# Optimization experiments

Hardware: AMD Instinct MI355X
Metric: run time of the kernel (lower is better)

The kernel has to match this reference:

```python
import jax, jax.numpy as jnp
import numpy as np

H = 32       # num_attention_heads
KV = 8       # num_key_value_heads
D = 128      # head_dim
HID = 4096   # hidden_size
EPS = 1e-6   # rms_norm_eps
BASE = 1000000.0  # rope_theta


def setup_inputs() -> dict:
    key = jax.random.key(0)
    ks = jax.random.split(key, 5)
    B, S = 1, 2048
    s = 0.02
    return {
        "x": jax.random.normal(ks[0], (B, S, HID), jnp.float32),
        "wq": jax.random.normal(ks[1], (H * D, HID), jnp.float32) * s,
        "wk": jax.random.normal(ks[2], (KV * D, HID), jnp.float32) * s,
        "wv": jax.random.normal(ks[3], (KV * D, HID), jnp.float32) * s,
        "wo": jax.random.normal(ks[4], (HID, H * D), jnp.float32) * s,
        "q_norm_w": jnp.ones((D,), jnp.float32),
        "k_norm_w": jnp.ones((D,), jnp.float32),
    }


def _rms(x, w):
    # F.rms_norm over last dim (head_dim), computed in fp32 then cast back
    x32 = x.astype(jnp.float32)
    y = x32 * jax.lax.rsqrt(jnp.mean(x32 * x32, axis=-1, keepdims=True) + EPS)
    return (y * w.astype(jnp.float32)).astype(x.dtype)


def _rope_tables(S, dtype):
    pair = jnp.arange(0, D, 2, dtype=jnp.float32)
    theta = 1.0 / (BASE ** (pair / D))                       # [D/2]
    ang = jnp.arange(S, dtype=jnp.float32)[:, None] * theta  # [S, D/2]
    ang = jnp.concatenate([ang, ang], axis=-1)               # [S, D]
    return jnp.cos(ang).astype(dtype), jnp.sin(ang).astype(dtype)


def _rope(x, cos, sin):
    # x: [B, H, S, D]; rotate_half convention (cat of two halves)
    half = D // 2
    rot = jnp.concatenate([-x[..., half:], x[..., :half]], axis=-1)
    return x * cos + rot * sin


def reference(x, wq, wk, wv, wo, q_norm_w, k_norm_w):
    B, S, _ = x.shape
    q = (x @ wq.T).reshape(B, S, H, D)
    k = (x @ wk.T).reshape(B, S, KV, D)
    v = (x @ wv.T).reshape(B, S, KV, D)
    q = _rms(q, q_norm_w).transpose(0, 2, 1, 3)   # [B, H, S, D]
    k = _rms(k, k_norm_w).transpose(0, 2, 1, 3)   # [B, KV, S, D]
    v = v.transpose(0, 2, 1, 3)                   # [B, KV, S, D]
    cos, sin = _rope_tables(S, x.dtype)
    q = _rope(q, cos, sin)
    k = _rope(k, cos, sin)
    # GQA: group Q heads over KV heads, causal SDPA
    G = H // KV
    qg = q.reshape(B, KV, G, S, D)
    scale = 1.0 / np.sqrt(D).astype(np.float32)
    scores = jnp.einsum('bkgsd,bktd->bkgst', qg, k) * scale  # [B,KV,G,S,S]
    causal = jnp.tril(jnp.ones((S, S), dtype=bool))
    scores = jnp.where(causal, scores, jnp.asarray(-jnp.inf, scores.dtype))
    p = jax.nn.softmax(scores, axis=-1)
    out = jnp.einsum('bkgst,bktd->bkgsd', p, v)               # [B,KV,G,S,D]
    out = out.reshape(B, H, S, D).transpose(0, 2, 1, 3).reshape(B, S, H * D)
    return out @ wo.T
```

## Files before the change

### kernel.cpp

```cpp
#include <hip/hip_runtime.h>
#include <hip/hip_bf16.h>

#define S_LEN   2048
#define HID_SZ  4096
#define NH      32
#define NKV     8
#define HD      128
#define EPS_F   1e-6f
#define QSCALE  0.1275174475f

typedef __attribute__((ext_vector_type(8))) short bf16x8;
typedef __attribute__((ext_vector_type(4))) float f32x4;

#define AS1(p) ((__attribute__((address_space(1))) void*)(p))
#define AS3(p) ((__attribute__((address_space(3))) void*)(p))

__device__ __forceinline__ short f2b(float f) {
  unsigned u = __builtin_bit_cast(unsigned, f);
  unsigned r = (u + 0x7fffu + ((u >> 16) & 1u)) >> 16;
  return (short)(unsigned short)r;
}
__device__ __forceinline__ float b2f(short s) {
  return __builtin_bit_cast(float, (unsigned)((unsigned short)s) << 16);
}

__global__ __launch_bounds__(256) void cvt_f32_bf16(const float* __restrict__ in,
                                                    short* __restrict__ out, int n4) {
  int i = blockIdx.x * 256 + threadIdx.x;
  if (i >= n4) return;
  float4 f = reinterpret_cast<const float4*>(in)[i];
  short4 o;
  o.x = f2b(f.x); o.y = f2b(f.y); o.z = f2b(f.z); o.w = f2b(f.w);
  reinterpret_cast<short4*>(out)[i] = o;
}

__global__ void rope_tables_k(float* __restrict__ cosT, float* __restrict__ sinT) {
  int s = blockIdx.x;
  int j = threadIdx.x;
  float theta = exp2f(-(float)(2 * j) * (19.931568569324174f / 128.0f));
  float ang = (float)s * theta;
  float sv, cv;
  sincosf(ang, &sv, &cv);
  cosT[s * 64 + j] = cv;
  sinT[s * 64 + j] = sv;
}

__global__ __launch_bounds__(256)
void rmsrope_k(const short* __restrict__ src, int srcCol,
               const float* __restrict__ w,
               const float* __restrict__ cosT, const float* __restrict__ sinT,
               short* __restrict__ dst, int heads, float outScale) {
  int gw   = blockIdx.x * 4 + (threadIdx.x >> 6);
  int lane = threadIdx.x & 63;
  int s = gw / heads;
  int h = gw - s * heads;
  const short* p = src + (size_t)s * 6144 + srcCol + h * HD;
  float x0 = b2f(p[lane]), x1 = b2f(p[lane + 64]);
  float ss = x0 * x0 + x1 * x1;
#pragma unroll
  for (int off = 1; off < 64; off <<= 1) ss += __shfl_xor(ss, off);
  float r = rsqrtf(ss * (1.0f / 128.0f) + EPS_F);
  float y0 = x0 * r * w[lane];
  float y1 = x1 * r * w[lane + 64];
  float c = cosT[s * 64 + lane], sn = sinT[s * 64 + lane];
  float o0 = (y0 * c - y1 * sn) * outScale;
  float o1 = (y1 * c + y0 * sn) * outScale;
  short* d = dst + ((size_t)h * S_LEN + s) * HD;
  d[lane]      = f2b(o0);
  d[lane + 64] = f2b(o1);
}

__global__ __launch_bounds__(256)
void vtrans_k(const short* __restrict__ qkvb, short* __restrict__ vt) {
  __shared__ short t[64][65];
  int s0 = blockIdx.x * 64;
  int d0 = blockIdx.y * 64;
  int kv = blockIdx.z;
  int j  = threadIdx.x & 63;
  int i0 = threadIdx.x >> 6;
#pragma unroll
  for (int r = 0; r < 16; ++r) {
    int i = i0 * 16 + r;
    t[i][j] = qkvb[(size_t)(s0 + i) * 6144 + 5120 + kv * HD + d0 + j];
  }
  __syncthreads();
#pragma unroll
  for (int r = 0; r < 16; ++r) {
    int i = i0 * 16 + r;
    vt[((size_t)kv * HD + d0 + i) * S_LEN + s0 + j] = t[j][i];
  }
}

template<bool BF16OUT>
__global__ __launch_bounds__(256)
void gemm_bt_k(const short* __restrict__ A, const short* __restrict__ B,
               void* __restrict__ Cv, int M, int N, int K) {
  __shared__ short As[128 * 32];
  __shared__ short Bs[128 * 32];
  int tid  = threadIdx.x;
  int lane = tid & 63;
  int wave = tid >> 6;
  int wr = wave >> 1, wc = wave & 1;
  int m0 = blockIdx.y * 128, n0 = blockIdx.x * 128;
  f32x4 acc[4][4] = {};
  int row16 = lane & 15;
  int kg    = (lane >> 4) << 3;
  int c0 = tid, c1 = tid + 256;
  const size_t rA0 = (size_t)(m0 + (c0 >> 2)) * K + ((c0 & 3) << 3);
  const size_t rA1 = (size_t)(m0 + (c1 >> 2)) * K + ((c1 & 3) << 3);
  const size_t rB0 = (size_t)(n0 + (c0 >> 2)) * K + ((c0 & 3) << 3);
  const size_t rB1 = (size_t)(n0 + (c1 >> 2)) * K + ((c1 & 3) << 3);
  for (int kt = 0; kt < K; kt += 32) {
    __builtin_amdgcn_global_load_lds(AS1(A + rA0 + kt), AS3(&As[c0 * 8]), 16, 0, 0);
    __builtin_amdgcn_global_load_lds(AS1(A + rA1 + kt), AS3(&As[c1 * 8]), 16, 0, 0);
    __builtin_amdgcn_global_load_lds(AS1(B + rB0 + kt), AS3(&Bs[c0 * 8]), 16, 0, 0);
    __builtin_amdgcn_global_load_lds(AS1(B + rB1 + kt), AS3(&Bs[c1 * 8]), 16, 0, 0);
    __syncthreads();
    bf16x8 af[4], bf[4];
#pragma unroll
    for (int i = 0; i < 4; ++i)
      af[i] = *reinterpret_cast<const bf16x8*>(&As[(wr * 64 + i * 16 + row16) * 32 + kg]);
#pragma unroll
    for (int j = 0; j < 4; ++j)
      bf[j] = *reinterpret_cast<const bf16x8*>(&Bs[(wc * 64 + j * 16 + row16) * 32 + kg]);
#pragma unroll
    for (int i = 0; i < 4; ++i)
#pragma unroll
      for (int j = 0; j < 4; ++j)
        acc[i][j] = __builtin_amdgcn_mfma_f32_16x16x32_bf16(af[i], bf[j], acc[i][j], 0, 0, 0);
    __syncthreads();
  }
  int rsub = (lane >> 4) << 2;
#pragma unroll
  for (int i = 0; i < 4; ++i)
#pragma unroll
    for (int j = 0; j < 4; ++j) {
      size_t base = (size_t)(m0 + wr * 64 + i * 16 + rsub) * N + (n0 + wc * 64 + j * 16 + row16);
#pragma unroll
      for (int reg = 0; reg < 4; ++reg) {
        if constexpr (BF16OUT) ((short*)Cv)[base + (size_t)reg * N] = f2b(acc[i][j][reg]);
        else                   ((float*)Cv)[base + (size_t)reg * N] = acc[i][j][reg];
      }
    }
}

__global__ __launch_bounds__(256)
void attn_k(const short* __restrict__ Qr, const short* __restrict__ Kr,
            const short* __restrict__ Vt, short* __restrict__ Ob) {
  constexpr int PP = 72;
  __shared__ short Kl[2][64 * 128];
  __shared__ short Vl[2][128 * 64];
  __shared__ short Pl[4][16 * PP];
  int pr  = blockIdx.x;
  int h   = blockIdx.y;
  int kvh = h >> 2;
  int tid = threadIdx.x, wave = tid >> 6, lane = tid & 63;
  int row16 = lane & 15, kg = (lane >> 4) << 3, rsub = (lane >> 4) << 2;
  int colb  = (lane >> 4) << 4;
  int swz   = (row16 & 7) << 4;

  const short* Kb = Kr + (size_t)kvh * S_LEN * HD;
  const short* Vb = Vt + (size_t)kvh * HD * S_LEN;

  int kso[4], vso[4], llo[4];
#pragma unroll
  for (int r = 0; r < 4; ++r) {
    int c = tid + r * 256;
    llo[r] = c * 8;
    int krow = c >> 4, ch = c & 15;
    int sch = (ch & 8) | ((ch ^ krow) & 7);
    kso[r] = krow * HD + sch * 8;
    int dr = c >> 3, vch = c & 7;
    int vsch = (vch ^ dr) & 7;
    vso[r] = dr * S_LEN + vsch * 8;
  }

#define STAGE(BUF, KT) do {                                                      \
    const short* Kt_ = Kb + (size_t)(KT) * 64 * HD;                              \
    const short* Vt_ = Vb + (KT) * 64;                                           \
    _Pragma("unroll")                                                            \
    for (int r_ = 0; r_ < 4; ++r_)                                               \
      __builtin_amdgcn_global_load_lds(AS1(Kt_ + kso[r_]),                       \
                                       AS3(&Kl[BUF][llo[r_]]), 16, 0, 0);        \
    _Pragma("unroll")                                                            \
    for (int r_ = 0; r_ < 4; ++r_)                                               \
      __builtin_amdgcn_global_load_lds(AS1(Vt_ + vso[r_]),                       \
                                       AS3(&Vl[BUF][llo[r_]]), 16, 0, 0);        \
  } while (0)

  STAGE(0, 0);

  for (int half = 0; half < 2; ++half) {
    int qb = half ? pr : (31 - pr);
    int qrow0 = qb * 64 + wave * 16;

    bf16x8 qf[4];
    {
      const short* qp = Qr + ((size_t)h * S_LEN + qrow0 + row16) * HD + kg;
#pragma unroll
      for (int ks = 0; ks < 4; ++ks)
        qf[ks] = *reinterpret_cast<const bf16x8*>(qp + ks * 32);
    }
    f32x4 o[8] = {};
    float mrow[4], lrow[4];
#pragma unroll
    for (int r = 0; r < 4; ++r) { mrow[r] = -3.0e38f; lrow[r] = 0.0f; }

    for (int kt = 0; kt <= qb; ++kt) {
      int cur = kt & 1;
      __syncthreads();
      if (kt < qb) STAGE(cur ^ 1, kt + 1);

      f32x4 s4[4];
      __builtin_amdgcn_s_setprio(1);
#pragma unroll
      for (int nc = 0; nc < 4; ++nc) {
        const char* rowp = (const char*)&Kl[cur][0] + (nc * 16 + row16) * 256;
        f32x4 a = {};
#pragma unroll
        for (int ks = 0; ks < 4; ++ks) {
          bf16x8 kf = *reinterpret_cast<const bf16x8*>(rowp + ((ks * 64 + colb) ^ swz));
          a = __builtin_amdgcn_mfma_f32_16x16x32_bf16(qf[ks], kf, a, 0, 0, 0);
        }
        s4[nc] = a;
      }
      __builtin_amdgcn_s_setprio(0);

      bool diag = (kt == qb);
      float mt[4] = {-3.0e38f, -3.0e38f, -3.0e38f, -3.0e38f};
#pragma unroll
      for (int nc = 0; nc < 4; ++nc)
#pragma unroll
        for (int reg = 0; reg < 4; ++reg) {
          float v = s4[nc][reg];
          if (diag && (kt * 64 + nc * 16 + row16) > (qrow0 + rsub + reg)) v = -3.0e38f;
          s4[nc][reg] = v;
          mt[reg] = fmaxf(mt[reg], v);
        }
#pragma unroll
      for (int reg = 0; reg < 4; ++reg)
#pragma unroll
        for (int off = 1; off < 16; off <<= 1)
          mt[reg] = fmaxf(mt[reg], __shfl_xor(mt[reg], off));

      float sc[4], st[4];
#pragma unroll
      for (int reg = 0; reg < 4; ++reg) {
        float mnew = fmaxf(mrow[reg], mt[reg]);
        sc[reg] = exp2f(mrow[reg] - mnew);
        mrow[reg] = mnew;
        st[reg] = 0.0f;
      }
#pragma unroll
      for (int nc = 0; nc < 4; ++nc)
#pragma unroll
        for (int reg = 0; reg < 4; ++reg) {
          float p = exp2f(s4[nc][reg] - mrow[reg]);
          s4[nc][reg] = p;
          st[reg] += p;
        }
#pragma unroll
      for (int reg = 0; reg < 4; ++reg) {
#pragma unroll
        for (int off = 1; off < 16; off <<= 1)
          st[reg] += __shfl_xor(st[reg], off);
        lrow[reg] = lrow[reg] * sc[reg] + st[reg];
      }
#pragma unroll
      for (int i = 0; i < 8; ++i) {
        f32x4 t = o[i];
        t[0] *= sc[0]; t[1] *= sc[1]; t[2] *= sc[2]; t[3] *= sc[3];
        o[i] = t;
      }

#pragma unroll
      for (int nc = 0; nc < 4; ++nc)
#pragma unroll
        for (int reg = 0; reg < 4; ++reg)
          Pl[wave][(rsub + reg) * PP + nc * 16 + row16] = f2b(s4[nc][reg]);

      __builtin_amdgcn_s_setprio(1);
#pragma unroll
      for (int ks = 0; ks < 2; ++ks) {
        bf16x8 pf = *reinterpret_cast<const bf16x8*>(&Pl[wave][row16 * PP + ks * 32 + kg]);
#pragma unroll
        for (int nc = 0; nc < 8; ++nc) {
          const char* rowp = (const char*)&Vl[cur][0] + (nc * 16 + row16) * 128;
          bf16x8 vf = *reinterpret_cast<const bf16x8*>(rowp + ((ks * 64 + colb) ^ swz));
          o[nc] = __builtin_amdgcn_mfma_f32_16x16x32_bf16(pf, vf, o[nc], 0, 0, 0);
        }
      }
      __builtin_amdgcn_s_setprio(0);
    }

    __syncthreads();
    if (half == 0) STAGE(0, 0);

#pragma unroll
    for (int nc = 0; nc < 8; ++nc)
#pragma unroll
      for (int reg = 0; reg < 4; ++reg) {
        float val = o[nc][reg] * (1.0f / lrow[reg]);
        int srow = qrow0 + rsub + reg;
        Ob[(size_t)srow * HID_SZ + h * HD + nc * 16 + row16] = f2b(val);
      }
  }
#undef STAGE
}

extern "C" void kernel_launch(void* const* d_in, const int* in_sizes, int n_in,
                              void* d_out, int out_size, void* d_ws, size_t ws_size,
                              hipStream_t stream) {
  const float* x   = (const float*)d_in[0];
  const float* wq  = (const float*)d_in[1];
  const float* wk  = (const float*)d_in[2];
  const float* wv  = (const float*)d_in[3];
  const float* wo  = (const float*)d_in[4];
  const float* qnw = (const float*)d_in[5];
  const float* knw = (const float*)d_in[6];
  float* out = (float*)d_out;

  char* ws = (char*)d_ws;
  short* xb    = (short*)(ws);
  short* attnb = (short*)(ws);
  short* wqkvb = (short*)(ws + (16ull  << 20));
  short* wob   = (short*)(ws + (16ull  << 20));
  short* qkvb  = (short*)(ws + (64ull  << 20));
  short* qr    = (short*)(ws + (88ull  << 20));
  short* kr    = (short*)(ws + (104ull << 20));
  short* vt    = (short*)(ws + (108ull << 20));
  float* cosT  = (float*)(ws + (112ull << 20));
  float* sinT  = (float*)(ws + (112ull << 20) + (512ull << 10));

  cvt_f32_bf16<<<8192,  256, 0, stream>>>(x,  xb,    2097152);
  cvt_f32_bf16<<<16384, 256, 0, stream>>>(wq, wqkvb,                       4194304);
  cvt_f32_bf16<<<4096,  256, 0, stream>>>(wk, wqkvb + (size_t)4096 * 4096, 1048576);
  cvt_f32_bf16<<<4096,  256, 0, stream>>>(wv, wqkvb + (size_t)5120 * 4096, 1048576);

  rope_tables_k<<<2048, 64, 0, stream>>>(cosT, sinT);

  gemm_bt_k<true><<<dim3(48, 16), 256, 0, stream>>>(xb, wqkvb, qkvb, 2048, 6144, 4096);

  cvt_f32_bf16<<<16384, 256, 0, stream>>>(wo, wob, 4194304);

  rmsrope_k<<<16384, 256, 0, stream>>>(qkvb, 0,    qnw, cosT, sinT, qr, NH,  QSCALE);
  rmsrope_k<<<4096,  256, 0, stream>>>(qkvb, 4096, knw, cosT, sinT, kr, NKV, 1.0f);
  vtrans_k<<<dim3(32, 2, 8), 256, 0, stream>>>(qkvb, vt);

  attn_k<<<dim3(16, 32), 256, 0, stream>>>(qr, kr, vt, attnb);

  gemm_bt_k<false><<<dim3(32, 16), 256, 0, stream>>>(attnb, wob, out, 2048, 4096, 4096);

  (void)in_sizes; (void)n_in; (void)out_size; (void)ws_size;
}
```

Measured before the change: 555.3 us.

## Add 256x256-tile double-buffered GEMM for fused QKV projection

Adds a new bf16 GEMM kernel using 256x256 output tiles, 512 threads, double-buffered LDS filled by direct global-to-LDS loads, and XOR-swizzled LDS reads. Prefetch of the next K-slice is split across two phases of the MFMA loop, and MFMA sections run at raised wave priority. The QKV projection now uses this kernel in place of the previous 128-tile GEMM. The goal is more data reuse per tile and better overlap of loads with compute. In exchange the grid shrinks to 192 blocks, which may underfill the CUs, and the larger tiles raise register and LDS pressure.

```diff
diff --git a/kernel.cpp b/kernel.cpp
--- a/kernel.cpp
+++ b/kernel.cpp
@@ -144,6 +144,131 @@
     }
 }
 
+__global__ __launch_bounds__(512, 2)
+void gemm256_k(const short* __restrict__ A, const short* __restrict__ B,
+               short* __restrict__ C, int M, int N, int K) {
+  __shared__ short As[2][256 * 64];
+  __shared__ short Bs[2][256 * 64];
+  int tid  = threadIdx.x;
+  int lane = tid & 63, wave = tid >> 6;
+  int wr = wave >> 2, wc = wave & 3;
+  int m0 = blockIdx.x * 256, n0 = blockIdx.y * 256;
+  int row16 = lane & 15;
+  int colB  = (lane >> 4) << 4;
+  f32x4 acc[8][4] = {};
+
+  int soff[4], ldst[4];
+#pragma unroll
+  for (int j = 0; j < 4; ++j) {
+    int c = j * 512 + tid;
+    int row = c >> 3, ch = c & 7;
+    int sch = ch ^ (((row >> 2) & 1) << 1);
+    soff[j] = row * K + sch * 8;
+    ldst[j] = c * 8;
+  }
+  const short* Ab = A + (size_t)m0 * K;
+  const short* Bb = B + (size_t)n0 * K;
+
+#pragma unroll
+  for (int j = 0; j < 4; ++j)
+    __builtin_amdgcn_global_load_lds(AS1(Ab + soff[j]), AS3(&As[0][ldst[j]]), 16, 0, 0);
+#pragma unroll
+  for (int j = 0; j < 4; ++j)
+    __builtin_amdgcn_global_load_lds(AS1(Bb + soff[j]), AS3(&Bs[0][ldst[j]]), 16, 0, 0);
+
+  const int NT = K >> 6;
+  for (int kt = 0; kt < NT; ++kt) {
+    int cb = kt & 1;
+    const short* Ac = &As[cb][0];
+    const short* Bc = &Bs[cb][0];
+    short* An = &As[cb ^ 1][0];
+    short* Bn = &Bs[cb ^ 1][0];
+    int koff = (kt + 1) << 6;
+
+    if (kt + 1 < NT) {
+      __builtin_amdgcn_global_load_lds(AS1(Ab + soff[0] + koff), AS3(&An[ldst[0]]), 16, 0, 0);
+      __builtin_amdgcn_global_load_lds(AS1(Ab + soff[1] + koff), AS3(&An[ldst[1]]), 16, 0, 0);
+      __builtin_amdgcn_global_load_lds(AS1(Bb + soff[0] + koff), AS3(&Bn[ldst[0]]), 16, 0, 0);
+      __builtin_amdgcn_global_load_lds(AS1(Bb + soff[1] + koff), AS3(&Bn[ldst[1]]), 16, 0, 0);
+      asm volatile("s_waitcnt vmcnt(4)" ::: "memory");
+    } else {
+      asm volatile("s_waitcnt vmcnt(0)" ::: "memory");
+    }
+    __builtin_amdgcn_s_barrier();
+    asm volatile("" ::: "memory");
+
+#define RD(BASE, R, KS)                                                          \
+    (*reinterpret_cast<const bf16x8*>((const char*)(BASE) +                      \
+        ((((R) * 128) + (KS) * 64 + colB) ^ ((((R) >> 2) & 1) << 5))))
+
+    bf16x8 bq[4], aq[4];
+#pragma unroll
+    for (int nj = 0; nj < 4; ++nj) bq[nj] = RD(Bc, wc * 64 + nj * 16 + row16, 0);
+#pragma unroll
+    for (int mi = 0; mi < 4; ++mi) aq[mi] = RD(Ac, wr * 128 + mi * 16 + row16, 0);
+    __builtin_amdgcn_s_setprio(1);
+#pragma unroll
+    for (int mi = 0; mi < 4; ++mi)
+#pragma unroll
+      for (int nj = 0; nj < 4; ++nj)
+        acc[mi][nj] = __builtin_amdgcn_mfma_f32_16x16x32_bf16(aq[mi], bq[nj], acc[mi][nj], 0, 0, 0);
+    __builtin_amdgcn_s_setprio(0);
+
+    if (kt + 1 < NT) {
+      __builtin_amdgcn_global_load_lds(AS1(Ab + soff[2] + koff), AS3(&An[ldst[2]]), 16, 0, 0);
+      __builtin_amdgcn_global_load_lds(AS1(Ab + soff[3] + koff), AS3(&An[ldst[3]]), 16, 0, 0);
+      __builtin_amdgcn_global_load_lds(AS1(Bb + soff[2] + koff), AS3(&Bn[ldst[2]]), 16, 0, 0);
+      __builtin_amdgcn_global_load_lds(AS1(Bb + soff[3] + koff), AS3(&Bn[ldst[3]]), 16, 0, 0);
+    }
+#pragma unroll
+    for (int mi = 0; mi < 4; ++mi) aq[mi] = RD(Ac, wr * 128 + (mi + 4) * 16 + row16, 0);
+    __builtin_amdgcn_s_setprio(1);
+#pragma unroll
+    for (int mi = 0; mi < 4; ++mi)
+#pragma unroll
+      for (int nj = 0; nj < 4; ++nj)
+        acc[mi + 4][nj] = __builtin_amdgcn_mfma_f32_16x16x32_bf16(aq[mi], bq[nj], acc[mi + 4][nj], 0, 0, 0);
+    __builtin_amdgcn_s_setprio(0);
+
+#pragma unroll
+    for (int nj = 0; nj < 4; ++nj) bq[nj] = RD(Bc, wc * 64 + nj * 16 + row16, 1);
+#pragma unroll
+    for (int mi = 0; mi < 4; ++mi) aq[mi] = RD(Ac, wr * 128 + mi * 16 + row16, 1);
+    __builtin_amdgcn_s_setprio(1);
+#pragma unroll
+    for (int mi = 0; mi < 4; ++mi)
+#pragma unroll
+      for (int nj = 0; nj < 4; ++nj)
+        acc[mi][nj] = __builtin_amdgcn_mfma_f32_16x16x32_bf16(aq[mi], bq[nj], acc[mi][nj], 0, 0, 0);
+    __builtin_amdgcn_s_setprio(0);
+
+#pragma unroll
+    for (int mi = 0; mi < 4; ++mi) aq[mi] = RD(Ac, wr * 128 + (mi + 4) * 16 + row16, 1);
+    __builtin_amdgcn_s_setprio(1);
+#pragma unroll
+    for (int mi = 0; mi < 4; ++mi)
+#pragma unroll
+      for (int nj = 0; nj < 4; ++nj)
+        acc[mi + 4][nj] = __builtin_amdgcn_mfma_f32_16x16x32_bf16(aq[mi], bq[nj], acc[mi + 4][nj], 0, 0, 0);
+    __builtin_amdgcn_s_setprio(0);
+    asm volatile("" ::: "memory");
+    __builtin_amdgcn_s_barrier();
+    asm volatile("" ::: "memory");
+#undef RD
+  }
+
+  int rsub = (lane >> 4) << 2;
+#pragma unroll
+  for (int mi = 0; mi < 8; ++mi)
+#pragma unroll
+    for (int nj = 0; nj < 4; ++nj) {
+      size_t base = (size_t)(m0 + wr * 128 + mi * 16 + rsub) * N + (n0 + wc * 64 + nj * 16 + row16);
+#pragma unroll
+      for (int reg = 0; reg < 4; ++reg)
+        C[base + (size_t)reg * N] = f2b(acc[mi][nj][reg]);
+    }
+}
+
 __global__ __launch_bounds__(256)
 void attn_k(const short* __restrict__ Qr, const short* __restrict__ Kr,
             const short* __restrict__ Vt, short* __restrict__ Ob) {
@@ -339,7 +464,7 @@
 
   rope_tables_k<<<2048, 64, 0, stream>>>(cosT, sinT);
 
-  gemm_bt_k<true><<<dim3(48, 16), 256, 0, stream>>>(xb, wqkvb, qkvb, 2048, 6144, 4096);
+  gemm256_k<<<dim3(8, 24), 512, 0, stream>>>(xb, wqkvb, qkvb, 2048, 6144, 4096);
 
   cvt_f32_bf16<<<16384, 256, 0, stream>>>(wo, wob, 4194304);
 
```

New measurement: 564.6 us. About the same (+1.7%).
